# Optimization experiments

Hardware: AMD Instinct MI355X
Metric: run time of the kernel (lower is better)

## Reference

```python
import jax, jax.numpy as jnp
import numpy as np

S_GRID = 7
B_BOX = 2
N_CLS = 20
N_CH = B_BOX * 5 + N_CLS  # 30
LAMBDA_OBJ = 5.0
LAMBDA_NOOBJ = 0.5
CI = np.array([4, 9])
BI = np.array([0, 1, 2, 3, 5, 6, 7, 8])


def setup_inputs() -> dict:
    key = jax.random.key(0)
    k1, k2 = jax.random.split(key)
    batch = 512
    P = jax.random.uniform(k1, (batch, S_GRID, S_GRID, N_CH), dtype=jnp.float32)
    T = jax.random.uniform(k2, (batch, S_GRID, S_GRID, N_CH), dtype=jnp.float32)
    # deterministic object mask: 1/8 of cells are 'object' cells (channel 4 == 1 exactly)
    cell_idx = jnp.arange(batch * S_GRID * S_GRID).reshape(batch, S_GRID, S_GRID)
    obj_mask = (cell_idx % 8 == 0).astype(jnp.float32)
    T = T.at[..., 4].set(obj_mask)
    return {"P": P, "T": T}


def _norm2dnorm(b, S):
    # (cx, cy, w, h) -> (x1, y1, x2, y2) with cx,cy divided by S
    xy = b[:, :2] / S
    wh = b[:, 2:]
    return jnp.concatenate([xy - 0.5 * wh, xy + 0.5 * wh], axis=-1)


def _iou_mat(b1, b2):
    # b1: (N,4), b2: (M,4) -> (N,M) IoU
    lt = jnp.maximum(b1[:, None, :2], b2[None, :, :2])
    rb = jnp.minimum(b1[:, None, 2:], b2[None, :, 2:])
    wh = jnp.clip(rb - lt, 0.0)
    inter = wh[..., 0] * wh[..., 1]
    a1 = (b1[:, 2] - b1[:, 0]) * (b1[:, 3] - b1[:, 1])
    a2 = (b2[:, 2] - b2[:, 0]) * (b2[:, 3] - b2[:, 1])
    return inter / (a1[:, None] + a2[None, :] - inter)


def reference(P, T):
    batch = P.shape[0]
    Pf = P.reshape(-1, N_CH)
    Tf = T.reshape(-1, N_CH)
    # masks computed on concrete data (static counts by construction)
    obj = np.asarray(Tf[:, 4] == 1.0)
    coord_idx = jnp.asarray(np.nonzero(obj)[0])
    noobj_idx = jnp.asarray(np.nonzero(~obj)[0])

    coordP = Pf[coord_idx]
    coordT = Tf[coord_idx]
    noobjP = Pf[noobj_idx]
    noobjT = Tf[noobj_idx]

    ClassP = coordP[:, B_BOX * 5:]
    ClassT = coordT[:, B_BOX * 5:]
    NoObjP = noobjP[:, CI].reshape(-1)
    NoObjT = noobjT[:, CI].reshape(-1)
    ConfP = coordP[:, CI].reshape(-1)          # (2*Ncoord,)
    BBoxP = coordP[:, BI].reshape(-1, 4)       # (2*Ncoord, 4)
    BBoxT = coordT[:, BI].reshape(-1, 4)

    # original torch code does this under no_grad -> stop_gradient
    BP = jax.lax.stop_gradient(_norm2dnorm(BBoxP, float(S_GRID)))
    BT = jax.lax.stop_gradient(_norm2dnorm(BBoxT, float(S_GRID)))
    M = _iou_mat(BP, BT)                       # (NSize, NSize)
    iou = jax.lax.stop_gradient(jnp.max(M, axis=0))
    idx = jnp.argmax(M, axis=0)                # best pred row per target column

    BPg = BP[idx]
    BTg = BT[idx]
    ConfPg = ConfP[idx]

    lossXY = jnp.sum((BPg[:, :2] - BTg[:, :2]) ** 2)
    lossWH = jnp.sum((jnp.sqrt(BPg[:, 2:]) - jnp.sqrt(BTg[:, 2:])) ** 2)
    lossObj = jnp.sum((ConfPg - iou) ** 2)
    lossNObj = jnp.sum((NoObjP - NoObjT) ** 2)
    lossClass = jnp.sum((ClassP - ClassT) ** 2)

    return (LAMBDA_OBJ * (lossXY + lossWH) + LAMBDA_NOOBJ * lossNObj + (lossObj + lossClass)) / batch
```

## Files before the change

kernel.cpp:

```cpp
#include <hip/hip_runtime.h>
#include <stdint.h>

#define S_GRID 7
#define N_CH 30
#define MAXB 8192
#define NTILE 32
#define NCHUNK 80
#define CHUNK_MAX 104


__global__ void k_init(float* __restrict__ acc, int* __restrict__ ctr, int* __restrict__ finalCtr) {
    if (threadIdx.x < 4)  acc[threadIdx.x] = 0.0f;
    if (threadIdx.x == 4) *ctr = 0;
    if (threadIdx.x == 5) *finalCtr = 0;
}

__global__ void k_prep(const float* __restrict__ P, const float* __restrict__ T, int ncell,
                       int* __restrict__ ctr,
                       float4* __restrict__ PB4, float4* __restrict__ BT4,
                       float* __restrict__ ConfP,
                       float* __restrict__ acc,
                       unsigned long long* __restrict__ maxkey) {
    int gid = blockIdx.x * 256 + threadIdx.x;
    if (gid < MAXB) maxkey[gid] = 0ull;

    int cell = gid;
    float2 pr[15], tr[15];
    if (cell < ncell) {
        const float2* p2 = (const float2*)(P + (size_t)cell * N_CH);
        const float2* t2 = (const float2*)(T + (size_t)cell * N_CH);
        #pragma unroll
        for (int k = 0; k < 15; ++k) { pr[k] = p2[k]; tr[k] = t2[k]; }
    } else {
        #pragma unroll
        for (int k = 0; k < 15; ++k) { pr[k] = make_float2(0.f, 0.f); tr[k] = make_float2(0.f, 0.f); }
    }
    bool obj = (cell < ncell) && (tr[2].x == 1.0f);

    int lane = threadIdx.x & 63;
    unsigned long long bm = __ballot(obj);
    int wcnt = __popcll(bm);
    int base = 0;
    if (lane == 0 && wcnt) base = atomicAdd(ctr, wcnt);
    base = __shfl(base, 0);

    float cls = 0.f, nob = 0.f;
    if (cell < ncell) {
        if (obj) {
            #pragma unroll
            for (int k = 5; k < 15; ++k) {
                float d0 = pr[k].x - tr[k].x, d1 = pr[k].y - tr[k].y;
                cls += d0 * d0 + d1 * d1;
            }
        } else {
            float d0 = pr[2].x - tr[2].x;
            float d1 = pr[4].y - tr[4].y;
            nob = d0 * d0 + d1 * d1;
        }
    }
    #pragma unroll
    for (int o = 32; o; o >>= 1) { cls += __shfl_down(cls, o); nob += __shfl_down(nob, o); }
    if (lane == 0) {
        if (cls != 0.f) atomicAdd(&acc[3], cls);
        if (nob != 0.f) atomicAdd(&acc[2], nob);
    }

    if (obj) {
        int rank = base + __popcll(bm & ((1ull << lane) - 1ull));
        float bx[2][5] = {
            { pr[0].x, pr[0].y, pr[1].x, pr[1].y, pr[2].x },
            { pr[2].y, pr[3].x, pr[3].y, pr[4].x, pr[4].y }
        };
        float tx[2][4] = {
            { tr[0].x, tr[0].y, tr[1].x, tr[1].y },
            { tr[2].y, tr[3].x, tr[3].y, tr[4].x }
        };
        #pragma unroll
        for (int bb = 0; bb < 2; ++bb) {
            int m = 2 * rank + bb;
            if (m < MAXB) {
                float cx = bx[bb][0] / (float)S_GRID, cy = bx[bb][1] / (float)S_GRID;
                float w = bx[bb][2], h = bx[bb][3];
                PB4[m] = make_float4(cx - 0.5f * w, cy - 0.5f * h, cx + 0.5f * w, cy + 0.5f * h);
                ConfP[m] = bx[bb][4];
                cx = tx[bb][0] / (float)S_GRID; cy = tx[bb][1] / (float)S_GRID;
                w = tx[bb][2]; h = tx[bb][3];
                BT4[m] = make_float4(cx - 0.5f * w, cy - 0.5f * h, cx + 0.5f * w, cy + 0.5f * h);
            }
        }
    }
}

__global__ __launch_bounds__(256, 8)
void k_match(const float4* __restrict__ PB4, const float4* __restrict__ BT4,
             const int* __restrict__ ctr,
             unsigned long long* __restrict__ maxkey) {
    __shared__ float4 sh[CHUNK_MAX];
    __shared__ float  sa[CHUNK_MAX];
    int nb = 2 * (*ctr); if (nb > MAXB) nb = MAXB;
    int tid = threadIdx.x;
    int j = blockIdx.x * 256 + tid;
    if (blockIdx.x * 256 >= nb) return;
    int c = blockIdx.y;
    int chunkLen = (((nb + NCHUNK - 1) / NCHUNK) + 7) & ~7;
    int i0 = c * chunkLen;
    int i1 = min(nb, i0 + chunkLen);
    if (i0 >= i1) return;

    int len = i1 - i0;
    int padded = (len + 7) & ~7;
    if (tid < padded) {
        float4 v = (tid < len) ? PB4[i0 + tid] : make_float4(3.f, 3.f, 3.f, 3.f);
        sh[tid] = v;
        sa[tid] = (v.z - v.x) * (v.w - v.y);
    }
    __syncthreads();

    float4 tb = BT4[min(j, nb - 1)];
    float ta = (tb.z - tb.x) * (tb.w - tb.y);
    float bI = -1.f, bS = 1.f;
    int bidx = i0;

    for (int kb = 0; kb < padded; kb += 8) {
        #define STEP(kk)  {                                                          \
            float4 bb = sh[kb + kk];                                                 \
            float aa = sa[kb + kk];                                                  \
            int sidx = i0 + kb + kk;                                                 \
            float t0, t1, t2, t3;                                                    \
            asm("v_max_f32 %0, %7, %11\n\t"    \
                "v_min_f32 %1, %9, %13\n\t"    \
                "v_sub_f32 %1, %1, %0\n\t"                                           \
                "v_max_f32 %1, 0, %1\n\t"      \
                "v_max_f32 %0, %8, %12\n\t"    \
                "v_min_f32 %2, %10, %14\n\t"   \
                "v_sub_f32 %2, %2, %0\n\t"                                           \
                "v_max_f32 %2, 0, %2\n\t"      \
                "v_mul_f32 %1, %1, %2\n\t"     \
                "v_add_f32 %0, %15, %16\n\t"   \
                "v_mul_f32 %2, %1, %4\n\t"     \
                "v_mul_f32 %3, %5, %0\n\t"     \
                "v_cmp_ngt_f32 vcc, %2, %3\n\t"  \
                "v_cndmask_b32 %5, %1, %5, vcc\n\t"  \
                "v_cndmask_b32 %4, %0, %4, vcc\n\t"  \
                "v_cndmask_b32 %6, %17, %6, vcc"     \
                : "=&v"(t0), "=&v"(t1), "=&v"(t2), "=&v"(t3),                        \
                  "+v"(bS), "+v"(bI), "+v"(bidx)                                     \
                : "v"(tb.x), "v"(tb.y), "v"(tb.z), "v"(tb.w),                        \
                  "v"(bb.x), "v"(bb.y), "v"(bb.z), "v"(bb.w),                        \
                  "v"(ta), "v"(aa), "v"(sidx)                                        \
                : "vcc");                                                            \
        }
        STEP(0) STEP(1) STEP(2) STEP(3) STEP(4) STEP(5) STEP(6) STEP(7)
        #undef STEP
    }

    if (j < nb) {
        float iou = (bI >= 0.f) ? (bI / (bS - bI)) : 0.f;
        unsigned long long key =
            ((unsigned long long)__float_as_uint(iou) << 32) |
            (unsigned long long)(0xFFFFFFFFu - (unsigned)bidx);
        atomicMax(&maxkey[j], key);
    }
}

__global__ void k_final(const float4* __restrict__ PB4, const float4* __restrict__ BT4,
                        const float* __restrict__ ConfP,
                        const int* __restrict__ ctr,
                        const unsigned long long* __restrict__ maxkey,
                        float* __restrict__ acc, int* __restrict__ finalCtr,
                        float* __restrict__ out, float inv_batch) {
    int nb = 2 * (*ctr); if (nb > MAXB) nb = MAXB;
    int tid = threadIdx.x;
    int j = blockIdx.x * 256 + tid;
    float sxywh = 0.f, sobj = 0.f;
    if (j < nb) {
        unsigned long long key = maxkey[j];
        float iou = __uint_as_float((unsigned)(key >> 32));
        unsigned idx = 0xFFFFFFFFu - (unsigned)(key & 0xFFFFFFFFull);
        float4 bp = PB4[idx];
        float4 bt = BT4[idx];
        float cp = ConfP[idx];
        float dx = bp.x - bt.x, dy = bp.y - bt.y;
        float dw = sqrtf(bp.z) - sqrtf(bt.z);
        float dh = sqrtf(bp.w) - sqrtf(bt.w);
        sxywh = dx * dx + dy * dy + dw * dw + dh * dh;
        float dob = cp - iou;
        sobj = dob * dob;
    }
    #pragma unroll
    for (int o = 32; o; o >>= 1) { sxywh += __shfl_down(sxywh, o); sobj += __shfl_down(sobj, o); }
    if ((tid & 63) == 0) {
        if (sxywh != 0.f) atomicAdd(&acc[0], sxywh);
        if (sobj != 0.f)  atomicAdd(&acc[1], sobj);
    }
    __syncthreads();
    if (tid == 0) {
        int old = __hip_atomic_fetch_add(finalCtr, 1, __ATOMIC_ACQ_REL, __HIP_MEMORY_SCOPE_AGENT);
        if (old == NTILE - 1) {
            float a0 = __hip_atomic_load(&acc[0], __ATOMIC_RELAXED, __HIP_MEMORY_SCOPE_AGENT);
            float a1 = __hip_atomic_load(&acc[1], __ATOMIC_RELAXED, __HIP_MEMORY_SCOPE_AGENT);
            float a2 = __hip_atomic_load(&acc[2], __ATOMIC_RELAXED, __HIP_MEMORY_SCOPE_AGENT);
            float a3 = __hip_atomic_load(&acc[3], __ATOMIC_RELAXED, __HIP_MEMORY_SCOPE_AGENT);
            out[0] = (5.0f * a0 + 0.5f * a2 + a1 + a3) * inv_batch;
        }
    }
}

extern "C" void kernel_launch(void* const* d_in, const int* in_sizes, int n_in,
                              void* d_out, int out_size, void* d_ws, size_t ws_size,
                              hipStream_t stream) {
    const float* P = (const float*)d_in[0];
    const float* T = (const float*)d_in[1];
    int ncell = in_sizes[0] / N_CH;
    int batch = ncell / (S_GRID * S_GRID);

    char* ws = (char*)d_ws;
    float* acc      = (float*)ws;
    int*   ctr      = (int*)(ws + 16);
    int*   finalCtr = (int*)(ws + 20);
    unsigned long long* maxkey = (unsigned long long*)(ws + 1024);
    float4* PB4  = (float4*)(ws + 66560);
    float4* BT4  = (float4*)(ws + 197632);
    float*  ConfP = (float*)(ws + 328704);

    int nblk = (ncell + 255) / 256;
    k_init <<<1, 64, 0, stream>>>(acc, ctr, finalCtr);
    k_prep <<<nblk, 256, 0, stream>>>(P, T, ncell, ctr, PB4, BT4, ConfP, acc, maxkey);
    dim3 g3(NTILE, NCHUNK);
    k_match<<<g3, 256, 0, stream>>>(PB4, BT4, ctr, maxkey);
    k_final<<<NTILE, 256, 0, stream>>>(PB4, BT4, ConfP, ctr, maxkey, acc, finalCtr,
                                       (float*)d_out, 1.0f / (float)batch);
}
```

Before: 51.08 us.

## Fuse final loss reduction into match kernel via per-tile last-block counters

```diff
diff --git a/kernel.cpp b/kernel.cpp
--- a/kernel.cpp
+++ b/kernel.cpp
@@ -2,6 +2,7 @@
 #include <stdint.h>
 
 #define S_GRID 7
+#define INV_S  0.14285714285714285f
 #define N_CH 30
 #define MAXB 8192
 #define NTILE 32
@@ -9,10 +10,12 @@
 #define CHUNK_MAX 104
 
 
-__global__ void k_init(float* __restrict__ acc, int* __restrict__ ctr, int* __restrict__ finalCtr) {
+__global__ void k_init(float* __restrict__ acc, int* __restrict__ ctr,
+                       int* __restrict__ finalCtr, int* __restrict__ tileCtr) {
     if (threadIdx.x < 4)  acc[threadIdx.x] = 0.0f;
     if (threadIdx.x == 4) *ctr = 0;
     if (threadIdx.x == 5) *finalCtr = 0;
+    if (threadIdx.x >= 8 && threadIdx.x < 8 + NTILE) tileCtr[threadIdx.x - 8] = 0;
 }
 
 __global__ void k_prep(const float* __restrict__ P, const float* __restrict__ T, int ncell,
@@ -79,11 +82,11 @@
         for (int bb = 0; bb < 2; ++bb) {
             int m = 2 * rank + bb;
             if (m < MAXB) {
-                float cx = bx[bb][0] / (float)S_GRID, cy = bx[bb][1] / (float)S_GRID;
+                float cx = bx[bb][0] * INV_S, cy = bx[bb][1] * INV_S;
                 float w = bx[bb][2], h = bx[bb][3];
                 PB4[m] = make_float4(cx - 0.5f * w, cy - 0.5f * h, cx + 0.5f * w, cy + 0.5f * h);
                 ConfP[m] = bx[bb][4];
-                cx = tx[bb][0] / (float)S_GRID; cy = tx[bb][1] / (float)S_GRID;
+                cx = tx[bb][0] * INV_S; cy = tx[bb][1] * INV_S;
                 w = tx[bb][2]; h = tx[bb][3];
                 BT4[m] = make_float4(cx - 0.5f * w, cy - 0.5f * h, cx + 0.5f * w, cy + 0.5f * h);
             }
@@ -93,88 +96,95 @@
 
 __global__ __launch_bounds__(256, 8)
 void k_match(const float4* __restrict__ PB4, const float4* __restrict__ BT4,
+             const float* __restrict__ ConfP,
              const int* __restrict__ ctr,
-             unsigned long long* __restrict__ maxkey) {
+             unsigned long long* __restrict__ maxkey,
+             int* __restrict__ tileCtr,
+             float* __restrict__ acc, int* __restrict__ finalCtr,
+             float* __restrict__ out, float inv_batch) {
     __shared__ float4 sh[CHUNK_MAX];
     __shared__ float  sa[CHUNK_MAX];
     int nb = 2 * (*ctr); if (nb > MAXB) nb = MAXB;
     int tid = threadIdx.x;
-    int j = blockIdx.x * 256 + tid;
-    if (blockIdx.x * 256 >= nb) return;
+    int jt = blockIdx.x;
+    int j = jt * 256 + tid;
+    if (jt * 256 >= nb) return;
     int c = blockIdx.y;
     int chunkLen = (((nb + NCHUNK - 1) / NCHUNK) + 7) & ~7;
     int i0 = c * chunkLen;
     int i1 = min(nb, i0 + chunkLen);
-    if (i0 >= i1) return;
-
-    int len = i1 - i0;
-    int padded = (len + 7) & ~7;
-    if (tid < padded) {
-        float4 v = (tid < len) ? PB4[i0 + tid] : make_float4(3.f, 3.f, 3.f, 3.f);
-        sh[tid] = v;
-        sa[tid] = (v.z - v.x) * (v.w - v.y);
-    }
+
+    if (i0 < i1) {
+        int len = i1 - i0;
+        int padded = (len + 7) & ~7;
+        if (tid < padded) {
+            float4 v = (tid < len) ? PB4[i0 + tid] : make_float4(3.f, 3.f, 3.f, 3.f);
+            sh[tid] = v;
+            sa[tid] = (v.z - v.x) * (v.w - v.y);
+        }
+        __syncthreads();
+
+        float4 tb = BT4[min(j, nb - 1)];
+        float ta = (tb.z - tb.x) * (tb.w - tb.y);
+        float bI = -1.f, bS = 1.f;
+        int bidx = i0;
+
+        for (int kb = 0; kb < padded; kb += 8) {
+            #define STEP(kk)  {                                                          \
+                float4 bb = sh[kb + kk];                                                 \
+                float aa = sa[kb + kk];                                                  \
+                int sidx = i0 + kb + kk;                                                 \
+                float t0, t1, t2, t3;                                                    \
+                asm("v_max_f32 %0, %7, %11\n\t"    \
+                    "v_min_f32 %1, %9, %13\n\t"    \
+                    "v_sub_f32 %1, %1, %0\n\t"                                           \
+                    "v_max_f32 %1, 0, %1\n\t"      \
+                    "v_max_f32 %0, %8, %12\n\t"    \
+                    "v_min_f32 %2, %10, %14\n\t"   \
+                    "v_sub_f32 %2, %2, %0\n\t"                                           \
+                    "v_max_f32 %2, 0, %2\n\t"      \
+                    "v_mul_f32 %1, %1, %2\n\t"     \
+                    "v_add_f32 %0, %15, %16\n\t"   \
+                    "v_mul_f32 %2, %1, %4\n\t"     \
+                    "v_mul_f32 %3, %5, %0\n\t"     \
+                    "v_cmp_ngt_f32 vcc, %2, %3\n\t"  \
+                    "v_cndmask_b32 %5, %1, %5, vcc\n\t"  \
+                    "v_cndmask_b32 %4, %0, %4, vcc\n\t"  \
+                    "v_cndmask_b32 %6, %17, %6, vcc"     \
+                    : "=&v"(t0), "=&v"(t1), "=&v"(t2), "=&v"(t3),                        \
+                      "+v"(bS), "+v"(bI), "+v"(bidx)                                     \
+                    : "v"(tb.x), "v"(tb.y), "v"(tb.z), "v"(tb.w),                        \
+                      "v"(bb.x), "v"(bb.y), "v"(bb.z), "v"(bb.w),                        \
+                      "v"(ta), "v"(aa), "v"(sidx)                                        \
+                    : "vcc");                                                            \
+            }
+            STEP(0) STEP(1) STEP(2) STEP(3) STEP(4) STEP(5) STEP(6) STEP(7)
+            #undef STEP
+        }
+
+        if (j < nb) {
+            float iou = (bI >= 0.f) ? (bI / (bS - bI)) : 0.f;
+            unsigned long long key =
+                ((unsigned long long)__float_as_uint(iou) << 32) |
+                (unsigned long long)(0xFFFFFFFFu - (unsigned)bidx);
+            atomicMax(&maxkey[j], key);
+        }
+    }
+
     __syncthreads();
-
-    float4 tb = BT4[min(j, nb - 1)];
-    float ta = (tb.z - tb.x) * (tb.w - tb.y);
-    float bI = -1.f, bS = 1.f;
-    int bidx = i0;
-
-    for (int kb = 0; kb < padded; kb += 8) {
-        #define STEP(kk)  {                                                          \
-            float4 bb = sh[kb + kk];                                                 \
-            float aa = sa[kb + kk];                                                  \
-            int sidx = i0 + kb + kk;                                                 \
-            float t0, t1, t2, t3;                                                    \
-            asm("v_max_f32 %0, %7, %11\n\t"    \
-                "v_min_f32 %1, %9, %13\n\t"    \
-                "v_sub_f32 %1, %1, %0\n\t"                                           \
-                "v_max_f32 %1, 0, %1\n\t"      \
-                "v_max_f32 %0, %8, %12\n\t"    \
-                "v_min_f32 %2, %10, %14\n\t"   \
-                "v_sub_f32 %2, %2, %0\n\t"                                           \
-                "v_max_f32 %2, 0, %2\n\t"      \
-                "v_mul_f32 %1, %1, %2\n\t"     \
-                "v_add_f32 %0, %15, %16\n\t"   \
-                "v_mul_f32 %2, %1, %4\n\t"     \
-                "v_mul_f32 %3, %5, %0\n\t"     \
-                "v_cmp_ngt_f32 vcc, %2, %3\n\t"  \
-                "v_cndmask_b32 %5, %1, %5, vcc\n\t"  \
-                "v_cndmask_b32 %4, %0, %4, vcc\n\t"  \
-                "v_cndmask_b32 %6, %17, %6, vcc"     \
-                : "=&v"(t0), "=&v"(t1), "=&v"(t2), "=&v"(t3),                        \
-                  "+v"(bS), "+v"(bI), "+v"(bidx)                                     \
-                : "v"(tb.x), "v"(tb.y), "v"(tb.z), "v"(tb.w),                        \
-                  "v"(bb.x), "v"(bb.y), "v"(bb.z), "v"(bb.w),                        \
-                  "v"(ta), "v"(aa), "v"(sidx)                                        \
-                : "vcc");                                                            \
-        }
-        STEP(0) STEP(1) STEP(2) STEP(3) STEP(4) STEP(5) STEP(6) STEP(7)
-        #undef STEP
-    }
-
-    if (j < nb) {
-        float iou = (bI >= 0.f) ? (bI / (bS - bI)) : 0.f;
-        unsigned long long key =
-            ((unsigned long long)__float_as_uint(iou) << 32) |
-            (unsigned long long)(0xFFFFFFFFu - (unsigned)bidx);
-        atomicMax(&maxkey[j], key);
-    }
-}
-
-__global__ void k_final(const float4* __restrict__ PB4, const float4* __restrict__ BT4,
-                        const float* __restrict__ ConfP,
-                        const int* __restrict__ ctr,
-                        const unsigned long long* __restrict__ maxkey,
-                        float* __restrict__ acc, int* __restrict__ finalCtr,
-                        float* __restrict__ out, float inv_batch) {
-    int nb = 2 * (*ctr); if (nb > MAXB) nb = MAXB;
-    int tid = threadIdx.x;
-    int j = blockIdx.x * 256 + tid;
+    __shared__ int shLast;
+    if (tid == 0) {
+        int old = __hip_atomic_fetch_add(&tileCtr[jt], 1, __ATOMIC_ACQ_REL,
+                                         __HIP_MEMORY_SCOPE_AGENT);
+        shLast = (old == NCHUNK - 1);
+    }
+    __syncthreads();
+    if (!shLast) return;
+
     float sxywh = 0.f, sobj = 0.f;
     if (j < nb) {
-        unsigned long long key = maxkey[j];
+        unsigned long long key = __hip_atomic_load(&maxkey[j], __ATOMIC_RELAXED,
+                                                   __HIP_MEMORY_SCOPE_AGENT);
         float iou = __uint_as_float((unsigned)(key >> 32));
         unsigned idx = 0xFFFFFFFFu - (unsigned)(key & 0xFFFFFFFFull);
         float4 bp = PB4[idx];
@@ -195,8 +205,9 @@
     }
     __syncthreads();
     if (tid == 0) {
+        int nActive = (nb + 255) / 256;
         int old = __hip_atomic_fetch_add(finalCtr, 1, __ATOMIC_ACQ_REL, __HIP_MEMORY_SCOPE_AGENT);
-        if (old == NTILE - 1) {
+        if (old == nActive - 1) {
             float a0 = __hip_atomic_load(&acc[0], __ATOMIC_RELAXED, __HIP_MEMORY_SCOPE_AGENT);
             float a1 = __hip_atomic_load(&acc[1], __ATOMIC_RELAXED, __HIP_MEMORY_SCOPE_AGENT);
             float a2 = __hip_atomic_load(&acc[2], __ATOMIC_RELAXED, __HIP_MEMORY_SCOPE_AGENT);
@@ -218,16 +229,16 @@
     float* acc      = (float*)ws;
     int*   ctr      = (int*)(ws + 16);
     int*   finalCtr = (int*)(ws + 20);
+    int*   tileCtr  = (int*)(ws + 64);
     unsigned long long* maxkey = (unsigned long long*)(ws + 1024);
     float4* PB4  = (float4*)(ws + 66560);
     float4* BT4  = (float4*)(ws + 197632);
     float*  ConfP = (float*)(ws + 328704);
 
     int nblk = (ncell + 255) / 256;
-    k_init <<<1, 64, 0, stream>>>(acc, ctr, finalCtr);
+    k_init <<<1, 64, 0, stream>>>(acc, ctr, finalCtr, tileCtr);
     k_prep <<<nblk, 256, 0, stream>>>(P, T, ncell, ctr, PB4, BT4, ConfP, acc, maxkey);
     dim3 g3(NTILE, NCHUNK);
-    k_match<<<g3, 256, 0, stream>>>(PB4, BT4, ctr, maxkey);
-    k_final<<<NTILE, 256, 0, stream>>>(PB4, BT4, ConfP, ctr, maxkey, acc, finalCtr,
-                                       (float*)d_out, 1.0f / (float)batch);
-}
+    k_match<<<g3, 256, 0, stream>>>(PB4, BT4, ConfP, ctr, maxkey, tileCtr,
+                                    acc, finalCtr, (float*)d_out, 1.0f / (float)batch);
+}
```

New measurement: 73.40 us. 43.7% more time.

## Replace global 64-bit atomicMax with per-chunk partial keys reduced in final kernel

Applied to the files above, without the earlier changes.

```diff
diff --git a/kernel.cpp b/kernel.cpp
--- a/kernel.cpp
+++ b/kernel.cpp
@@ -2,10 +2,11 @@
 #include <stdint.h>
 
 #define S_GRID 7
+#define INV_S  0.14285714285714285f
 #define N_CH 30
 #define MAXB 8192
 #define NTILE 32
-#define NCHUNK 80
+#define NCHUNK 64
 #define CHUNK_MAX 104
 
 
@@ -19,11 +20,8 @@
                        int* __restrict__ ctr,
                        float4* __restrict__ PB4, float4* __restrict__ BT4,
                        float* __restrict__ ConfP,
-                       float* __restrict__ acc,
-                       unsigned long long* __restrict__ maxkey) {
+                       float* __restrict__ acc) {
     int gid = blockIdx.x * 256 + threadIdx.x;
-    if (gid < MAXB) maxkey[gid] = 0ull;
-
     int cell = gid;
     float2 pr[15], tr[15];
     if (cell < ncell) {
@@ -79,11 +77,11 @@
         for (int bb = 0; bb < 2; ++bb) {
             int m = 2 * rank + bb;
             if (m < MAXB) {
-                float cx = bx[bb][0] / (float)S_GRID, cy = bx[bb][1] / (float)S_GRID;
+                float cx = bx[bb][0] * INV_S, cy = bx[bb][1] * INV_S;
                 float w = bx[bb][2], h = bx[bb][3];
                 PB4[m] = make_float4(cx - 0.5f * w, cy - 0.5f * h, cx + 0.5f * w, cy + 0.5f * h);
                 ConfP[m] = bx[bb][4];
-                cx = tx[bb][0] / (float)S_GRID; cy = tx[bb][1] / (float)S_GRID;
+                cx = tx[bb][0] * INV_S; cy = tx[bb][1] * INV_S;
                 w = tx[bb][2]; h = tx[bb][3];
                 BT4[m] = make_float4(cx - 0.5f * w, cy - 0.5f * h, cx + 0.5f * w, cy + 0.5f * h);
             }
@@ -94,7 +92,7 @@
 __global__ __launch_bounds__(256, 8)
 void k_match(const float4* __restrict__ PB4, const float4* __restrict__ BT4,
              const int* __restrict__ ctr,
-             unsigned long long* __restrict__ maxkey) {
+             unsigned long long* __restrict__ pkeys) {
     __shared__ float4 sh[CHUNK_MAX];
     __shared__ float  sa[CHUNK_MAX];
     int nb = 2 * (*ctr); if (nb > MAXB) nb = MAXB;
@@ -159,14 +157,14 @@
         unsigned long long key =
             ((unsigned long long)__float_as_uint(iou) << 32) |
             (unsigned long long)(0xFFFFFFFFu - (unsigned)bidx);
-        atomicMax(&maxkey[j], key);
+        pkeys[(size_t)c * MAXB + j] = key;
     }
 }
 
 __global__ void k_final(const float4* __restrict__ PB4, const float4* __restrict__ BT4,
                         const float* __restrict__ ConfP,
                         const int* __restrict__ ctr,
-                        const unsigned long long* __restrict__ maxkey,
+                        const unsigned long long* __restrict__ pkeys,
                         float* __restrict__ acc, int* __restrict__ finalCtr,
                         float* __restrict__ out, float inv_batch) {
     int nb = 2 * (*ctr); if (nb > MAXB) nb = MAXB;
@@ -174,7 +172,14 @@
     int j = blockIdx.x * 256 + tid;
     float sxywh = 0.f, sobj = 0.f;
     if (j < nb) {
-        unsigned long long key = maxkey[j];
+        int chunkLen = (((nb + NCHUNK - 1) / NCHUNK) + 7) & ~7;
+        unsigned long long key = 0;
+        #pragma unroll 4
+        for (int c = 0; c < NCHUNK; ++c) {
+            if (c * chunkLen >= nb) break;
+            unsigned long long k2 = pkeys[(size_t)c * MAXB + j];
+            if (k2 > key) key = k2;
+        }
         float iou = __uint_as_float((unsigned)(key >> 32));
         unsigned idx = 0xFFFFFFFFu - (unsigned)(key & 0xFFFFFFFFull);
         float4 bp = PB4[idx];
@@ -218,16 +223,16 @@
     float* acc      = (float*)ws;
     int*   ctr      = (int*)(ws + 16);
     int*   finalCtr = (int*)(ws + 20);
-    unsigned long long* maxkey = (unsigned long long*)(ws + 1024);
-    float4* PB4  = (float4*)(ws + 66560);
-    float4* BT4  = (float4*)(ws + 197632);
-    float*  ConfP = (float*)(ws + 328704);
+    float4* PB4  = (float4*)(ws + 1024);
+    float4* BT4  = (float4*)(ws + 132096);
+    float*  ConfP = (float*)(ws + 263168);
+    unsigned long long* pkeys = (unsigned long long*)(ws + 299008);
 
     int nblk = (ncell + 255) / 256;
     k_init <<<1, 64, 0, stream>>>(acc, ctr, finalCtr);
-    k_prep <<<nblk, 256, 0, stream>>>(P, T, ncell, ctr, PB4, BT4, ConfP, acc, maxkey);
+    k_prep <<<nblk, 256, 0, stream>>>(P, T, ncell, ctr, PB4, BT4, ConfP, acc);
     dim3 g3(NTILE, NCHUNK);
-    k_match<<<g3, 256, 0, stream>>>(PB4, BT4, ctr, maxkey);
-    k_final<<<NTILE, 256, 0, stream>>>(PB4, BT4, ConfP, ctr, maxkey, acc, finalCtr,
+    k_match<<<g3, 256, 0, stream>>>(PB4, BT4, ctr, pkeys);
+    k_final<<<NTILE, 256, 0, stream>>>(PB4, BT4, ConfP, ctr, pkeys, acc, finalCtr,
                                        (float*)d_out, 1.0f / (float)batch);
 }
```

New measurement: 58.85 us. 1.15x slower.
